# Kernel optimization log

Hardware: AMD Instinct MI355X
Metric: run time of the kernel (lower is better)

## Reference

```python
import jax, jax.numpy as jnp
import numpy as np

IN_F = 8192
OUT_F = 8192
GROUP = 128
BATCH = 32


def dequantize(packed, scale, zero):
    """Unpack int4 pairs from uint8 and dequantize per 128-wide group.

    packed: [n_groups/2, 128] uint8 (hi nibble -> first half rows, lo nibble -> second half)
    scale, zero: [n_groups, 1] float32, broadcast over the 128 group columns.
    Returns dense weight [OUT_F, IN_F].
    """
    p = packed.astype(jnp.int32)
    hi = ((p >> 4) & 15).astype(jnp.float32)
    lo = (p & 15).astype(jnp.float32)
    w = jnp.concatenate([hi, lo], axis=0)          # [n_groups, 128]
    w = (w - zero) * scale                          # per-group affine dequant
    return w.reshape(OUT_F, IN_F)


def setup_inputs() -> dict:
    key = jax.random.key(0)
    k1, k2, k3, k4, k5 = jax.random.split(key, 5)
    n_groups = OUT_F * IN_F // GROUP
    x = jax.random.normal(k1, (BATCH, IN_F), dtype=jnp.float32)
    packed = jax.random.randint(k2, (n_groups // 2, GROUP), 0, 256, dtype=jnp.int32).astype(jnp.uint8)
    scale = jax.random.uniform(k3, (n_groups, 1), dtype=jnp.float32, minval=0.005, maxval=0.02)
    zero = jax.random.uniform(k4, (n_groups, 1), dtype=jnp.float32, minval=0.0, maxval=15.0)
    bias = jax.random.normal(k5, (OUT_F,), dtype=jnp.float32) * 0.01
    return {"x": x, "packed": packed, "scale": scale, "zero": zero, "bias": bias}


def reference(x, packed, scale, zero, bias):
    W = dequantize(packed, scale, zero)             # [OUT_F, IN_F]
    return x @ W.T + bias                            # [BATCH, OUT_F]
```

## Files before the change

kernel.cpp:

```cpp
#include <hip/hip_runtime.h>

#define IN_F 8192
#define OUT_F 8192
#define BATCH 32
#define HALFG ((OUT_F / 2) * (IN_F / 128))
#define NFRAG_HALF 16384

typedef __bf16 bf16x8 __attribute__((ext_vector_type(8)));
typedef __bf16 bf16x4 __attribute__((ext_vector_type(4)));
typedef float f32x4 __attribute__((ext_vector_type(4)));

union ABFrag { bf16x8 v; uint2 h[2]; int4 i4; };

__global__ __launch_bounds__(256) void xcvt_kernel(const float* __restrict__ x,
                                                   bf16x8* __restrict__ xc) {
    int t = blockIdx.x * 256 + threadIdx.x;
    int r = t & 15;
    int q = (t >> 4) & 3;
    int k32 = (t >> 6) & 255;
    int half = t >> 14;
    int b = half * 16 + r;
    int kb = k32 * 32 + q * 4;
    float4 x0 = *(const float4*)(x + (size_t)b * IN_F + kb);
    float4 x1 = *(const float4*)(x + (size_t)b * IN_F + kb + 16);
    bf16x8 o;
    o[0] = (__bf16)x0.x; o[1] = (__bf16)x0.y; o[2] = (__bf16)x0.z; o[3] = (__bf16)x0.w;
    o[4] = (__bf16)x1.x; o[5] = (__bf16)x1.y; o[6] = (__bf16)x1.z; o[7] = (__bf16)x1.w;
    xc[t] = o;
}

__global__ __launch_bounds__(256) void bias_init_kernel(const float4* __restrict__ bias,
                                                        float4* __restrict__ out) {
    int i = blockIdx.x * 256 + threadIdx.x;
    out[i] = bias[i & 2047];
}

template <int KSPLIT, bool FAST>
__global__ __launch_bounds__(256, 4) void qgemm_kernel(
    const float* __restrict__ xf, const bf16x8* __restrict__ xc,
    const int* __restrict__ packed, const float* __restrict__ scale,
    const float* __restrict__ zero, float* __restrict__ outp) {
    constexpr int KCHUNK = IN_F / KSPLIT;
    constexpr int NKG = KCHUNK / 128;
    const int w = threadIdx.x >> 6;
    const int lane = threadIdx.x & 63;
    const int r = lane & 15;
    const int q = lane >> 4;
    const int nb = blockIdx.x;
    const int ks = blockIdx.y;
    const int pr = nb * 64 + w * 16 + r;
    const int kbase = ks * KCHUNK;

    f32x4 acc[2][2] = {{{0.f, 0.f, 0.f, 0.f}, {0.f, 0.f, 0.f, 0.f}},
                       {{0.f, 0.f, 0.f, 0.f}, {0.f, 0.f, 0.f, 0.f}}};

    const int* pk = packed + (size_t)pr * IN_F;

    const int ghi = pr * 64 + (kbase >> 7);
    float4 sh = *(const float4*)(scale + ghi);
    float4 zh = *(const float4*)(zero + ghi);
    float4 sl = *(const float4*)(scale + ghi + HALFG);
    float4 zl = *(const float4*)(zero + ghi + HALFG);
    float4 zsh, zsl;
    zsh.x = -zh.x * sh.x; zsh.y = -zh.y * sh.y; zsh.z = -zh.z * sh.z; zsh.w = -zh.w * sh.w;
    zsl.x = -zl.x * sl.x; zsl.y = -zl.y * sl.y; zsl.z = -zl.z * sl.z; zsl.w = -zl.w * sl.w;
    const float sh_a[4] = {sh.x, sh.y, sh.z, sh.w};
    const float zsh_a[4] = {zsh.x, zsh.y, zsh.z, zsh.w};
    const float sl_a[4] = {sl.x, sl.y, sl.z, sl.w};
    const float zsl_a[4] = {zsl.x, zsl.y, zsl.z, zsl.w};

#pragma unroll
    for (int kg = 0; kg < NKG; ++kg) {
        const float s_hi = sh_a[kg], zs_hi = zsh_a[kg];
        const float s_lo = sl_a[kg], zs_lo = zsl_a[kg];
#pragma unroll
        for (int ki = 0; ki < 4; ++ki) {
            const int k32g = ks * (KCHUNK / 32) + kg * 4 + ki;
            const int k0 = kbase + kg * 128 + ki * 32 + q * 4;
            int4 p0 = *(const int4*)(pk + k0);
            int4 p1 = *(const int4*)(pk + k0 + 16);
            ABFrag a0, a1;
            if (FAST) {
                a0.i4 = *(const int4*)(xc + (size_t)k32g * 64 + lane);
                a1.i4 = *(const int4*)(xc + (size_t)NFRAG_HALF + (size_t)k32g * 64 + lane);
            } else {
                float4 x00 = *(const float4*)(xf + (size_t)r * IN_F + k0);
                float4 x01 = *(const float4*)(xf + (size_t)r * IN_F + k0 + 16);
                float4 x10 = *(const float4*)(xf + (size_t)(16 + r) * IN_F + k0);
                float4 x11 = *(const float4*)(xf + (size_t)(16 + r) * IN_F + k0 + 16);
                a0.v[0] = (__bf16)x00.x; a0.v[1] = (__bf16)x00.y;
                a0.v[2] = (__bf16)x00.z; a0.v[3] = (__bf16)x00.w;
                a0.v[4] = (__bf16)x01.x; a0.v[5] = (__bf16)x01.y;
                a0.v[6] = (__bf16)x01.z; a0.v[7] = (__bf16)x01.w;
                a1.v[0] = (__bf16)x10.x; a1.v[1] = (__bf16)x10.y;
                a1.v[2] = (__bf16)x10.z; a1.v[3] = (__bf16)x10.w;
                a1.v[4] = (__bf16)x11.x; a1.v[5] = (__bf16)x11.y;
                a1.v[6] = (__bf16)x11.z; a1.v[7] = (__bf16)x11.w;
            }
            int pp[8] = {p0.x, p0.y, p0.z, p0.w, p1.x, p1.y, p1.z, p1.w};
            bf16x8 bhi, blo;
#pragma unroll
            for (int j = 0; j < 8; ++j) {
                bhi[j] = (__bf16)fmaf((float)(pp[j] >> 4), s_hi, zs_hi);
                blo[j] = (__bf16)fmaf((float)(pp[j] & 15), s_lo, zs_lo);
            }
            acc[0][0] = __builtin_amdgcn_mfma_f32_16x16x32_bf16(a0.v, bhi, acc[0][0], 0, 0, 0);
            acc[1][0] = __builtin_amdgcn_mfma_f32_16x16x32_bf16(a1.v, bhi, acc[1][0], 0, 0, 0);
            acc[0][1] = __builtin_amdgcn_mfma_f32_16x16x32_bf16(a0.v, blo, acc[0][1], 0, 0, 0);
            acc[1][1] = __builtin_amdgcn_mfma_f32_16x16x32_bf16(a1.v, blo, acc[1][1], 0, 0, 0);
        }
    }

#pragma unroll
    for (int bt = 0; bt < 2; ++bt) {
#pragma unroll
        for (int hl = 0; hl < 2; ++hl) {
            const int o = nb * 64 + w * 16 + r + hl * (OUT_F / 2);
#pragma unroll
            for (int j = 0; j < 4; ++j) {
                const int b = bt * 16 + q * 4 + j;
                if (FAST) {
                    outp[(size_t)ks * (BATCH * OUT_F) + (size_t)b * OUT_F + o] = acc[bt][hl][j];
                } else {
                    atomicAdd(&outp[(size_t)b * OUT_F + o], acc[bt][hl][j]);
                }
            }
        }
    }
}

template <int KSPLIT>
__global__ __launch_bounds__(256) void reduce_kernel(const float4* __restrict__ part,
                                                     const float4* __restrict__ bias,
                                                     float4* __restrict__ out) {
    int i = blockIdx.x * 256 + threadIdx.x;
    float4 s = bias[i & 2047];
#pragma unroll
    for (int k = 0; k < KSPLIT; ++k) {
        float4 p = part[(size_t)k * (BATCH * OUT_F / 4) + i];
        s.x += p.x; s.y += p.y; s.z += p.z; s.w += p.w;
    }
    out[i] = s;
}

extern "C" void kernel_launch(void* const* d_in, const int* in_sizes, int n_in,
                              void* d_out, int out_size, void* d_ws, size_t ws_size,
                              hipStream_t stream) {
    (void)in_sizes; (void)n_in; (void)out_size;
    const float* x = (const float*)d_in[0];
    const int* packed = (const int*)d_in[1];
    const float* scale = (const float*)d_in[2];
    const float* zero = (const float*)d_in[3];
    const float* bias = (const float*)d_in[4];
    float* out = (float*)d_out;

    constexpr int KSPLIT = 16;
    const size_t part_bytes = (size_t)KSPLIT * BATCH * OUT_F * sizeof(float);
    const size_t xc_bytes = (size_t)2 * NFRAG_HALF * 16;
    const size_t need = part_bytes + xc_bytes;

    if (ws_size >= need) {
        float* part = (float*)d_ws;
        bf16x8* xc = (bf16x8*)((char*)d_ws + part_bytes);
        xcvt_kernel<<<128, 256, 0, stream>>>(x, xc);
        qgemm_kernel<KSPLIT, true><<<dim3(OUT_F / 2 / 64, KSPLIT), 256, 0, stream>>>(
            nullptr, xc, packed, scale, zero, part);
        reduce_kernel<KSPLIT><<<256, 256, 0, stream>>>((const float4*)part,
                                                       (const float4*)bias, (float4*)out);
    } else {
        bias_init_kernel<<<256, 256, 0, stream>>>((const float4*)bias, (float4*)out);
        qgemm_kernel<KSPLIT, false><<<dim3(OUT_F / 2 / 64, KSPLIT), 256, 0, stream>>>(
            x, nullptr, packed, scale, zero, out);
    }
}
```

Before: 39.38 us.

## Switch to fp16 MFMA with magic-number int4 dequant and prefetched nontemporal weight loads

Moves activations and dequantized weights from bf16 to fp16 and builds the weight fragments with the 0x6400 magic-number trick. Each 4-bit value is OR'd into an fp16 mantissa and dequantized with packed half2 subtract and FMA, replacing per-element int-to-float conversion, fp32 FMA and bf16 conversion. The fast path also double-buffers the packed-weight loads one iteration ahead using nontemporal loads, to hide memory latency. In exchange, scale and zero-offset are rounded to fp16, so there is some risk of precision loss and of fp16 overflow for larger inputs.

```diff
diff --git a/kernel.cpp b/kernel.cpp
--- a/kernel.cpp
+++ b/kernel.cpp
@@ -6,14 +6,24 @@
 #define HALFG ((OUT_F / 2) * (IN_F / 128))
 #define NFRAG_HALF 16384
 
-typedef __bf16 bf16x8 __attribute__((ext_vector_type(8)));
-typedef __bf16 bf16x4 __attribute__((ext_vector_type(4)));
+typedef _Float16 f16x2 __attribute__((ext_vector_type(2)));
+typedef _Float16 f16x8 __attribute__((ext_vector_type(8)));
 typedef float f32x4 __attribute__((ext_vector_type(4)));
-
-union ABFrag { bf16x8 v; uint2 h[2]; int4 i4; };
+typedef int i32x4 __attribute__((ext_vector_type(4)));
+
+union AFrag { f16x8 v; i32x4 i4; };
+union BFrag { f16x8 v; unsigned int u[4]; };
+union F16x2U { f16x2 v; unsigned int u; };
+
+__device__ inline f16x2 dq_pair(unsigned int h_bits, f16x2 s2, f16x2 zs2) {
+    F16x2U h; h.u = h_bits;
+    const f16x2 c1024 = {(_Float16)1024.0f, (_Float16)1024.0f};
+    f16x2 n = h.v - c1024;
+    return n * s2 + zs2;
+}
 
 __global__ __launch_bounds__(256) void xcvt_kernel(const float* __restrict__ x,
-                                                   bf16x8* __restrict__ xc) {
+                                                   f16x8* __restrict__ xc) {
     int t = blockIdx.x * 256 + threadIdx.x;
     int r = t & 15;
     int q = (t >> 4) & 3;
@@ -23,9 +33,9 @@
     int kb = k32 * 32 + q * 4;
     float4 x0 = *(const float4*)(x + (size_t)b * IN_F + kb);
     float4 x1 = *(const float4*)(x + (size_t)b * IN_F + kb + 16);
-    bf16x8 o;
-    o[0] = (__bf16)x0.x; o[1] = (__bf16)x0.y; o[2] = (__bf16)x0.z; o[3] = (__bf16)x0.w;
-    o[4] = (__bf16)x1.x; o[5] = (__bf16)x1.y; o[6] = (__bf16)x1.z; o[7] = (__bf16)x1.w;
+    f16x8 o;
+    o[0] = (_Float16)x0.x; o[1] = (_Float16)x0.y; o[2] = (_Float16)x0.z; o[3] = (_Float16)x0.w;
+    o[4] = (_Float16)x1.x; o[5] = (_Float16)x1.y; o[6] = (_Float16)x1.z; o[7] = (_Float16)x1.w;
     xc[t] = o;
 }
 
@@ -37,11 +47,12 @@
 
 template <int KSPLIT, bool FAST>
 __global__ __launch_bounds__(256, 4) void qgemm_kernel(
-    const float* __restrict__ xf, const bf16x8* __restrict__ xc,
+    const float* __restrict__ xf, const f16x8* __restrict__ xc,
     const int* __restrict__ packed, const float* __restrict__ scale,
     const float* __restrict__ zero, float* __restrict__ outp) {
     constexpr int KCHUNK = IN_F / KSPLIT;
     constexpr int NKG = KCHUNK / 128;
+    constexpr int NIT = NKG * 4;
     const int w = threadIdx.x >> 6;
     const int lane = threadIdx.x & 63;
     const int r = lane & 15;
@@ -61,53 +72,103 @@
     float4 zh = *(const float4*)(zero + ghi);
     float4 sl = *(const float4*)(scale + ghi + HALFG);
     float4 zl = *(const float4*)(zero + ghi + HALFG);
-    float4 zsh, zsl;
-    zsh.x = -zh.x * sh.x; zsh.y = -zh.y * sh.y; zsh.z = -zh.z * sh.z; zsh.w = -zh.w * sh.w;
-    zsl.x = -zl.x * sl.x; zsl.y = -zl.y * sl.y; zsl.z = -zl.z * sl.z; zsl.w = -zl.w * sl.w;
     const float sh_a[4] = {sh.x, sh.y, sh.z, sh.w};
-    const float zsh_a[4] = {zsh.x, zsh.y, zsh.z, zsh.w};
+    const float zh_a[4] = {zh.x, zh.y, zh.z, zh.w};
     const float sl_a[4] = {sl.x, sl.y, sl.z, sl.w};
-    const float zsl_a[4] = {zsl.x, zsl.y, zsl.z, zsl.w};
-
-#pragma unroll
-    for (int kg = 0; kg < NKG; ++kg) {
-        const float s_hi = sh_a[kg], zs_hi = zsh_a[kg];
-        const float s_lo = sl_a[kg], zs_lo = zsl_a[kg];
-#pragma unroll
-        for (int ki = 0; ki < 4; ++ki) {
-            const int k32g = ks * (KCHUNK / 32) + kg * 4 + ki;
-            const int k0 = kbase + kg * 128 + ki * 32 + q * 4;
-            int4 p0 = *(const int4*)(pk + k0);
-            int4 p1 = *(const int4*)(pk + k0 + 16);
-            ABFrag a0, a1;
-            if (FAST) {
-                a0.i4 = *(const int4*)(xc + (size_t)k32g * 64 + lane);
-                a1.i4 = *(const int4*)(xc + (size_t)NFRAG_HALF + (size_t)k32g * 64 + lane);
-            } else {
-                float4 x00 = *(const float4*)(xf + (size_t)r * IN_F + k0);
-                float4 x01 = *(const float4*)(xf + (size_t)r * IN_F + k0 + 16);
-                float4 x10 = *(const float4*)(xf + (size_t)(16 + r) * IN_F + k0);
-                float4 x11 = *(const float4*)(xf + (size_t)(16 + r) * IN_F + k0 + 16);
-                a0.v[0] = (__bf16)x00.x; a0.v[1] = (__bf16)x00.y;
-                a0.v[2] = (__bf16)x00.z; a0.v[3] = (__bf16)x00.w;
-                a0.v[4] = (__bf16)x01.x; a0.v[5] = (__bf16)x01.y;
-                a0.v[6] = (__bf16)x01.z; a0.v[7] = (__bf16)x01.w;
-                a1.v[0] = (__bf16)x10.x; a1.v[1] = (__bf16)x10.y;
-                a1.v[2] = (__bf16)x10.z; a1.v[3] = (__bf16)x10.w;
-                a1.v[4] = (__bf16)x11.x; a1.v[5] = (__bf16)x11.y;
-                a1.v[6] = (__bf16)x11.z; a1.v[7] = (__bf16)x11.w;
-            }
-            int pp[8] = {p0.x, p0.y, p0.z, p0.w, p1.x, p1.y, p1.z, p1.w};
-            bf16x8 bhi, blo;
-#pragma unroll
-            for (int j = 0; j < 8; ++j) {
-                bhi[j] = (__bf16)fmaf((float)(pp[j] >> 4), s_hi, zs_hi);
-                blo[j] = (__bf16)fmaf((float)(pp[j] & 15), s_lo, zs_lo);
-            }
-            acc[0][0] = __builtin_amdgcn_mfma_f32_16x16x32_bf16(a0.v, bhi, acc[0][0], 0, 0, 0);
-            acc[1][0] = __builtin_amdgcn_mfma_f32_16x16x32_bf16(a1.v, bhi, acc[1][0], 0, 0, 0);
-            acc[0][1] = __builtin_amdgcn_mfma_f32_16x16x32_bf16(a0.v, blo, acc[0][1], 0, 0, 0);
-            acc[1][1] = __builtin_amdgcn_mfma_f32_16x16x32_bf16(a1.v, blo, acc[1][1], 0, 0, 0);
+    const float zl_a[4] = {zl.x, zl.y, zl.z, zl.w};
+    f16x2 s2h[4], zs2h[4], s2l[4], zs2l[4];
+#pragma unroll
+    for (int kg = 0; kg < 4; ++kg) {
+        _Float16 s = (_Float16)sh_a[kg];
+        _Float16 zs = (_Float16)(-zh_a[kg] * sh_a[kg]);
+        s2h[kg][0] = s; s2h[kg][1] = s; zs2h[kg][0] = zs; zs2h[kg][1] = zs;
+        s = (_Float16)sl_a[kg];
+        zs = (_Float16)(-zl_a[kg] * sl_a[kg]);
+        s2l[kg][0] = s; s2l[kg][1] = s; zs2l[kg][0] = zs; zs2l[kg][1] = zs;
+    }
+
+    if (FAST) {
+        i32x4 pb0[2], pb1[2];
+        {
+            const int k0 = kbase + q * 4;
+            pb0[0] = __builtin_nontemporal_load((const i32x4*)(pk + k0));
+            pb1[0] = __builtin_nontemporal_load((const i32x4*)(pk + k0 + 16));
+        }
+#pragma unroll
+        for (int it = 0; it < NIT; ++it) {
+            const int kg = it >> 2;
+            if (it + 1 < NIT) {
+                const int k0n = kbase + (it + 1) * 32 + q * 4;
+                pb0[(it + 1) & 1] = __builtin_nontemporal_load((const i32x4*)(pk + k0n));
+                pb1[(it + 1) & 1] = __builtin_nontemporal_load((const i32x4*)(pk + k0n + 16));
+            }
+            const int k32g = ks * NIT + it;
+            AFrag a0, a1;
+            a0.i4 = *(const i32x4*)(xc + (size_t)k32g * 64 + lane);
+            a1.i4 = *(const i32x4*)(xc + (size_t)NFRAG_HALF + (size_t)k32g * 64 + lane);
+            const i32x4 p0 = pb0[it & 1];
+            const i32x4 p1 = pb1[it & 1];
+            const unsigned int tt[4] = {
+                (unsigned int)p0[0] | ((unsigned int)p0[1] << 16),
+                (unsigned int)p0[2] | ((unsigned int)p0[3] << 16),
+                (unsigned int)p1[0] | ((unsigned int)p1[1] << 16),
+                (unsigned int)p1[2] | ((unsigned int)p1[3] << 16)};
+            BFrag bhi, blo;
+#pragma unroll
+            for (int pi = 0; pi < 4; ++pi) {
+                unsigned int hlo = (tt[pi] & 0x000F000Fu) | 0x64006400u;
+                unsigned int hhi = ((tt[pi] >> 4) & 0x000F000Fu) | 0x64006400u;
+                F16x2U wl, wh;
+                wl.v = dq_pair(hlo, s2l[kg], zs2l[kg]);
+                wh.v = dq_pair(hhi, s2h[kg], zs2h[kg]);
+                blo.u[pi] = wl.u;
+                bhi.u[pi] = wh.u;
+            }
+            acc[0][0] = __builtin_amdgcn_mfma_f32_16x16x32_f16(a0.v, bhi.v, acc[0][0], 0, 0, 0);
+            acc[1][0] = __builtin_amdgcn_mfma_f32_16x16x32_f16(a1.v, bhi.v, acc[1][0], 0, 0, 0);
+            acc[0][1] = __builtin_amdgcn_mfma_f32_16x16x32_f16(a0.v, blo.v, acc[0][1], 0, 0, 0);
+            acc[1][1] = __builtin_amdgcn_mfma_f32_16x16x32_f16(a1.v, blo.v, acc[1][1], 0, 0, 0);
+        }
+    } else {
+#pragma unroll
+        for (int it = 0; it < NIT; ++it) {
+            const int kg = it >> 2;
+            const int k0 = kbase + it * 32 + q * 4;
+            i32x4 p0 = *(const i32x4*)(pk + k0);
+            i32x4 p1 = *(const i32x4*)(pk + k0 + 16);
+            float4 x00 = *(const float4*)(xf + (size_t)r * IN_F + k0);
+            float4 x01 = *(const float4*)(xf + (size_t)r * IN_F + k0 + 16);
+            float4 x10 = *(const float4*)(xf + (size_t)(16 + r) * IN_F + k0);
+            float4 x11 = *(const float4*)(xf + (size_t)(16 + r) * IN_F + k0 + 16);
+            AFrag a0, a1;
+            a0.v[0] = (_Float16)x00.x; a0.v[1] = (_Float16)x00.y;
+            a0.v[2] = (_Float16)x00.z; a0.v[3] = (_Float16)x00.w;
+            a0.v[4] = (_Float16)x01.x; a0.v[5] = (_Float16)x01.y;
+            a0.v[6] = (_Float16)x01.z; a0.v[7] = (_Float16)x01.w;
+            a1.v[0] = (_Float16)x10.x; a1.v[1] = (_Float16)x10.y;
+            a1.v[2] = (_Float16)x10.z; a1.v[3] = (_Float16)x10.w;
+            a1.v[4] = (_Float16)x11.x; a1.v[5] = (_Float16)x11.y;
+            a1.v[6] = (_Float16)x11.z; a1.v[7] = (_Float16)x11.w;
+            const unsigned int tt[4] = {
+                (unsigned int)p0[0] | ((unsigned int)p0[1] << 16),
+                (unsigned int)p0[2] | ((unsigned int)p0[3] << 16),
+                (unsigned int)p1[0] | ((unsigned int)p1[1] << 16),
+                (unsigned int)p1[2] | ((unsigned int)p1[3] << 16)};
+            BFrag bhi, blo;
+#pragma unroll
+            for (int pi = 0; pi < 4; ++pi) {
+                unsigned int hlo = (tt[pi] & 0x000F000Fu) | 0x64006400u;
+                unsigned int hhi = ((tt[pi] >> 4) & 0x000F000Fu) | 0x64006400u;
+                F16x2U wl, wh;
+                wl.v = dq_pair(hlo, s2l[kg], zs2l[kg]);
+                wh.v = dq_pair(hhi, s2h[kg], zs2h[kg]);
+                blo.u[pi] = wl.u;
+                bhi.u[pi] = wh.u;
+            }
+            acc[0][0] = __builtin_amdgcn_mfma_f32_16x16x32_f16(a0.v, bhi.v, acc[0][0], 0, 0, 0);
+            acc[1][0] = __builtin_amdgcn_mfma_f32_16x16x32_f16(a1.v, bhi.v, acc[1][0], 0, 0, 0);
+            acc[0][1] = __builtin_amdgcn_mfma_f32_16x16x32_f16(a0.v, blo.v, acc[0][1], 0, 0, 0);
+            acc[1][1] = __builtin_amdgcn_mfma_f32_16x16x32_f16(a1.v, blo.v, acc[1][1], 0, 0, 0);
         }
     }
 
@@ -161,7 +222,7 @@
 
     if (ws_size >= need) {
         float* part = (float*)d_ws;
-        bf16x8* xc = (bf16x8*)((char*)d_ws + part_bytes);
+        f16x8* xc = (f16x8*)((char*)d_ws + part_bytes);
         xcvt_kernel<<<128, 256, 0, stream>>>(x, xc);
         qgemm_kernel<KSPLIT, true><<<dim3(OUT_F / 2 / 64, KSPLIT), 256, 0, stream>>>(
             nullptr, xc, packed, scale, zero, part);
```

After: 59.25 us. 1.5x slower.
